# Performance work log

Measured on AMD Instinct MI355X. Metric: run time of the kernel, lower is better.

The kernel has to match this reference:

```python
import jax, jax.numpy as jnp
import numpy as np

KERNEL = 25  # hard-coded moving-average kernel in the torch Model
HID = 128


def moving_avg(x):
    # x: [B, L, C]; edge-pad (KERNEL-1)//2 on each side along time, then mean over window
    p = (KERNEL - 1) // 2
    front = jnp.repeat(x[:, 0:1, :], p, axis=1)
    end = jnp.repeat(x[:, -1:, :], p, axis=1)
    xp = jnp.concatenate([front, x, end], axis=1)  # [B, L+2p, C]
    cs = jnp.cumsum(xp, axis=1)
    cs = jnp.concatenate([jnp.zeros_like(cs[:, :1, :]), cs], axis=1)
    return (cs[:, KERNEL:, :] - cs[:, :-KERNEL, :]) / KERNEL  # [B, L, C]


def memory_enhance(repres, memory):
    # repres: [N, 128], memory: [F, 128]
    attention = jax.nn.softmax(jnp.einsum('nd,fd->nf', repres, memory), axis=1)
    output = jnp.einsum('nf,fd->nd', attention, memory)
    return jnp.concatenate([output, repres], axis=1)  # [N, 256]


def setup_inputs() -> dict:
    key = jax.random.key(0)
    ks = jax.random.split(key, 12)
    B, L, C, P, M = 128, 720, 321, 336, 512
    s = lambda k, shape, fan: jax.random.normal(k, shape, jnp.float32) * (1.0 / np.sqrt(fan))
    return {
        'x': jax.random.normal(ks[0], (B, L, C), jnp.float32),
        'W_s1': s(ks[1], (HID, L), L), 'b_s1': jnp.zeros((HID,), jnp.float32),
        'W_s2': s(ks[2], (P, 2 * HID), 2 * HID), 'b_s2': jnp.zeros((P,), jnp.float32),
        'W_t1': s(ks[3], (HID, L), L), 'b_t1': jnp.zeros((HID,), jnp.float32),
        'W_t2': s(ks[4], (P, 2 * HID), 2 * HID), 'b_t2': jnp.zeros((P,), jnp.float32),
        'mem_S': s(ks[5], (M, HID), HID),
        'mem_T': s(ks[6], (M, HID), HID),
    }


def reference(x, W_s1, b_s1, W_s2, b_s2, W_t1, b_t1, W_t2, b_t2, mem_S, mem_T):
    B, L, C = x.shape
    trend = moving_avg(x)                 # [B, L, C]
    seasonal = x - trend
    seasonal = jnp.transpose(seasonal, (0, 2, 1))  # [B, C, L]
    trend = jnp.transpose(trend, (0, 2, 1))

    def branch(init, W1, b1, mem, W2, b2):
        r = jax.nn.sigmoid(jnp.einsum('bcl,hl->bch', init, W1) + b1)  # [B, C, 128]
        r = r.reshape(-1, HID)
        r = memory_enhance(r, mem)                                    # [N, 256]
        r = r.reshape(B, C, 2 * HID)
        return jnp.einsum('bcd,pd->bcp', r, W2) + b2                  # [B, C, P]

    seasonal_out = branch(seasonal, W_s1, b_s1, mem_S, W_s2, b_s2)
    trend_out = branch(trend, W_t1, b_t1, mem_T, W_t2, b_t2)
    return jnp.transpose(seasonal_out + trend_out, (0, 2, 1))  # [B, P, C]
```

## Files before the change

### kernel.cpp

```cpp
#include <hip/hip_runtime.h>
#include <math.h>

#define BB 128
#define LL 720
#define CC 321
#define HH 128
#define PP 336
#define MM 512
#define LPAD 736

typedef __attribute__((ext_vector_type(8))) short bf16x8;
typedef __attribute__((ext_vector_type(4))) float f32x4;

__device__ __forceinline__ short f2bf(float x) {
  unsigned u = __builtin_bit_cast(unsigned, x);
  u = (u + 0x7FFFu + ((u >> 16) & 1u)) >> 16;
  return (short)u;
}

__device__ __forceinline__ bf16x8 ldfrag(const short* p) {
  short4 a = *(const short4*)p;
  short4 b = *(const short4*)(p + 16);
  bf16x8 r;
  r[0] = a.x; r[1] = a.y; r[2] = a.z; r[3] = a.w;
  r[4] = b.x; r[5] = b.y; r[6] = b.z; r[7] = b.w;
  return r;
}

__device__ __forceinline__ int4 stage_chunk(const short* g) {
  int2 lo = *(const int2*)g;
  int2 hi = *(const int2*)(g + 16);
  int4 r;
  r.x = lo.x; r.y = lo.y; r.z = hi.x; r.w = hi.y;
  return r;
}

__device__ __forceinline__ bf16x8 ldsfragP(const short* tile, int h, int lg) {
  return *(const bf16x8*)&tile[h * 40 + lg * 8];
}

__device__ __forceinline__ bf16x8 ldsfragR(const short* tile, int h, int lg) {
  int2 lo = *(const int2*)&tile[h * 40 + lg * 4];
  int2 hi = *(const int2*)&tile[h * 40 + lg * 4 + 16];
  union { int2 v[2]; bf16x8 f; } u;
  u.v[0] = lo;
  u.v[1] = hi;
  return u.f;
}

__device__ __forceinline__ void gload_lds16(const short* g, short* l) {
  __builtin_amdgcn_global_load_lds(
      (const __attribute__((address_space(1))) unsigned int*)g,
      (__attribute__((address_space(3))) unsigned int*)l, 16, 0, 0);
}

__global__ void weff_kernel(const float* __restrict__ Ws1,
                            const float* __restrict__ Wt1,
                            short* __restrict__ WsT,
                            short* __restrict__ WtT) {
  int idx = blockIdx.x * 256 + threadIdx.x;
  if (idx >= HH * LPAD) return;
  int j = idx % LPAD, h = idx / LPAD;
  if (j >= LL) { WsT[idx] = 0; WtT[idx] = 0; return; }
  float ss = 0.f, st = 0.f;
  if (j == 0) {
    for (int l = 0; l <= 12; ++l) {
      float w = 13.f - (float)l;
      ss += w * Ws1[h * LL + l];
      st += w * Wt1[h * LL + l];
    }
  } else if (j == LL - 1) {
    for (int d = 0; d <= 12; ++d) {
      float w = 13.f - (float)d;
      ss += w * Ws1[h * LL + LL - 1 - d];
      st += w * Wt1[h * LL + LL - 1 - d];
    }
  } else {
    int lo = j - 12 < 0 ? 0 : j - 12;
    int hi = j + 12 > LL - 1 ? LL - 1 : j + 12;
    for (int l = lo; l <= hi; ++l) {
      ss += Ws1[h * LL + l];
      st += Wt1[h * LL + l];
    }
  }
  ss *= (1.f / 25.f);
  st *= (1.f / 25.f);
  WsT[idx] = f2bf(Ws1[h * LL + j] - ss);
  WtT[idx] = f2bf(st);
}

__global__ void memstage_kernel(const float* __restrict__ memS,
                                const float* __restrict__ memT,
                                short* __restrict__ stgS,
                                short* __restrict__ stgT) {
  int e = blockIdx.x * 256 + threadIdx.x;
  int br = e >> 14;
  int s = e & 16383;
  const float* src = br ? memT : memS;
  short* dst = br ? stgT : stgS;
  int tt = s >> 11;
  int c = s & 2047;
  int row = c >> 4, slot = c & 15;
  int sp = slot ^ (row & 7);
  int k = sp >> 2, lg = sp & 3;
  int ft = tt >> 1;
  short out[8];
  if ((tt & 1) == 0) {
    const float* r0 = src + (size_t)(ft * 128 + row) * 128 + k * 32 + lg * 4;
#pragma unroll
    for (int j = 0; j < 4; ++j) {
      out[j] = f2bf(r0[j]);
      out[j + 4] = f2bf(r0[16 + j]);
    }
  } else {
    int fbase = ft * 128 + k * 32 + lg * 4;
#pragma unroll
    for (int j = 0; j < 4; ++j) {
      out[j] = f2bf(src[(size_t)(fbase + j) * 128 + row]);
      out[j + 4] = f2bf(src[(size_t)(fbase + 16 + j) * 128 + row]);
    }
  }
  short4 a = make_short4(out[0], out[1], out[2], out[3]);
  short4 b = make_short4(out[4], out[5], out[6], out[7]);
  *(short4*)&dst[(size_t)s * 8] = a;
  *(short4*)&dst[(size_t)s * 8 + 4] = b;
}

__global__ void w2cvt_kernel(const float* __restrict__ Ws2,
                             const float* __restrict__ Wt2,
                             const float* __restrict__ bs2,
                             const float* __restrict__ bt2,
                             short* __restrict__ W2b, float* __restrict__ b2) {
  int i = blockIdx.x * 256 + threadIdx.x;
  if (i < PP) b2[i] = bs2[i] + bt2[i];
  if (i >= PP * 512) return;
  int p = i >> 9, k = i & 511;
  float v = (k < 256) ? Ws2[p * 256 + k] : Wt2[p * 256 + (k - 256)];
  W2b[i] = f2bf(v);
}

__global__ __launch_bounds__(256) void gemm1_mfma(
    const float* __restrict__ x,
    const short* __restrict__ WsT, const short* __restrict__ WtT,
    const float* __restrict__ bs1, const float* __restrict__ bt1,
    short* __restrict__ r2s, short* __restrict__ r2t) {
  __shared__ __align__(16) short wlds[2][2][128 * 40];
  int tid = threadIdx.x;
  int w = tid >> 6, l = tid & 63, lr = l & 15, lg = l >> 4;
  int ngrp = w >> 1, hhalf = w & 1;
  int n0 = blockIdx.x * 64 + ngrp * 32 + lr;
  int n1 = n0 + 16;
  int b0 = n0 / CC, c0 = n0 - b0 * CC;
  int b1 = n1 / CC, c1 = n1 - b1 * CC;
  const float* xb0 = x + (size_t)b0 * (LL * CC) + c0;
  const float* xb1 = x + (size_t)b1 * (LL * CC) + c1;

  int rowA = tid >> 2, cqA = tid & 3;
  int rowB = (tid + 256) >> 2, cqB = tid & 3;
  const short* gSA = WsT + rowA * LPAD + cqA * 8;
  const short* gSB = WsT + rowB * LPAD + cqB * 8;
  const short* gTA = WtT + rowA * LPAD + cqA * 8;
  const short* gTB = WtT + rowB * LPAD + cqB * 8;
  int dA = rowA * 40 + cqA * 8;
  int dB = rowB * 40 + cqB * 8;

  f32x4 acc[2][4][2];
#pragma unroll
  for (int br = 0; br < 2; ++br)
#pragma unroll
    for (int i = 0; i < 4; ++i)
#pragma unroll
      for (int rt = 0; rt < 2; ++rt) acc[br][i][rt] = (f32x4){0.f, 0.f, 0.f, 0.f};

  {
    int4 sA = *(const int4*)gSA;
    int4 sB = *(const int4*)gSB;
    int4 tA = *(const int4*)gTA;
    int4 tB = *(const int4*)gTB;
    *(int4*)&wlds[0][0][dA] = sA;
    *(int4*)&wlds[0][0][dB] = sB;
    *(int4*)&wlds[0][1][dA] = tA;
    *(int4*)&wlds[0][1][dB] = tB;
  }
  float xc0[8], xc1[8];
#pragma unroll
  for (int j = 0; j < 4; ++j) {
    int k1 = lg * 4 + j, k2 = k1 + 16;
    xc0[j] = xb0[(size_t)k1 * CC];
    xc0[j + 4] = xb0[(size_t)k2 * CC];
    xc1[j] = xb1[(size_t)k1 * CC];
    xc1[j + 4] = xb1[(size_t)k2 * CC];
  }
  __syncthreads();

  int hb = hhalf * 64;
  int cur = 0;
  for (int step = 0; step < 23; ++step) {
    int4 nSA = {0, 0, 0, 0}, nSB = nSA, nTA = nSA, nTB = nSA;
    float xn0[8] = {0.f}, xn1[8] = {0.f};
    if (step < 22) {
      int ko = (step + 1) * 32;
      nSA = *(const int4*)(gSA + ko);
      nSB = *(const int4*)(gSB + ko);
      nTA = *(const int4*)(gTA + ko);
      nTB = *(const int4*)(gTB + ko);
#pragma unroll
      for (int j = 0; j < 4; ++j) {
        int k1 = ko + lg * 4 + j;
        int k2 = k1 + 16;
        bool ok = k2 < LL;
        xn0[j] = xb0[(size_t)k1 * CC];
        xn0[j + 4] = ok ? xb0[(size_t)k2 * CC] : 0.f;
        xn1[j] = xb1[(size_t)k1 * CC];
        xn1[j + 4] = ok ? xb1[(size_t)k2 * CC] : 0.f;
      }
    }

    bf16x8 bx0, bx1;
#pragma unroll
    for (int j = 0; j < 8; ++j) {
      bx0[j] = f2bf(xc0[j]);
      bx1[j] = f2bf(xc1[j]);
    }

    const short* tS = &wlds[cur][0][0];
    const short* tT = &wlds[cur][1][0];
#pragma unroll
    for (int ht = 0; ht < 4; ++ht) {
      int h = hb + ht * 16 + lr;
      bf16x8 aS = ldsfragR(tS, h, lg);
      bf16x8 aT = ldsfragR(tT, h, lg);
      acc[0][ht][0] =
          __builtin_amdgcn_mfma_f32_16x16x32_bf16(aS, bx0, acc[0][ht][0], 0, 0, 0);
      acc[0][ht][1] =
          __builtin_amdgcn_mfma_f32_16x16x32_bf16(aS, bx1, acc[0][ht][1], 0, 0, 0);
      acc[1][ht][0] =
          __builtin_amdgcn_mfma_f32_16x16x32_bf16(aT, bx0, acc[1][ht][0], 0, 0, 0);
      acc[1][ht][1] =
          __builtin_amdgcn_mfma_f32_16x16x32_bf16(aT, bx1, acc[1][ht][1], 0, 0, 0);
    }

    if (step < 22) {
      short* bS = &wlds[cur ^ 1][0][0];
      short* bT = &wlds[cur ^ 1][1][0];
      *(int4*)&bS[dA] = nSA;
      *(int4*)&bS[dB] = nSB;
      *(int4*)&bT[dA] = nTA;
      *(int4*)&bT[dB] = nTB;
    }
    __syncthreads();
#pragma unroll
    for (int j = 0; j < 8; ++j) {
      xc0[j] = xn0[j];
      xc1[j] = xn1[j];
    }
    cur ^= 1;
  }

#pragma unroll
  for (int rt = 0; rt < 2; ++rt) {
    int n = rt ? n1 : n0;
    short* rowS = r2s + (size_t)n * 256 + 128;
    short* rowT = r2t + (size_t)n * 256 + 128;
#pragma unroll
    for (int ht = 0; ht < 4; ++ht) {
      int h = hb + ht * 16 + lg * 4;
      float4 bS = *(const float4*)&bs1[h];
      float4 bT = *(const float4*)&bt1[h];
      const float* pbS = &bS.x;
      const float* pbT = &bT.x;
      short4 ss, st;
      short* ps = &ss.x;
      short* pt = &st.x;
#pragma unroll
      for (int j = 0; j < 4; ++j) {
        ps[j] = f2bf(1.f / (1.f + __expf(-(acc[0][ht][rt][j] + pbS[j]))));
        pt[j] = f2bf(1.f / (1.f + __expf(-(acc[1][ht][rt][j] + pbT[j]))));
      }
      *(short4*)&rowS[h] = ss;
      *(short4*)&rowT[h] = st;
    }
  }
}

__global__ __launch_bounds__(256) void memenh_mfma(
    const short* __restrict__ stgS, const short* __restrict__ stgT,
    short* __restrict__ r2s, short* __restrict__ r2t) {
  int br = blockIdx.y;
  const short* stg = br ? stgT : stgS;
  short* r2 = br ? r2t : r2s;

  __shared__ __align__(16) short buf[2][16384];
  int tid = threadIdx.x;
  int l = tid & 63, lr = l & 15, lg = l >> 4;
  int wbase = tid & 192;
  int n = blockIdx.x * 64 + (tid >> 6) * 16 + lr;

  bf16x8 brag[4];
  {
    const short* rb = r2 + (size_t)n * 256 + 128;
#pragma unroll
    for (int k = 0; k < 4; ++k) brag[k] = ldfrag(rb + k * 32 + lg * 4);
  }

#define STAGE(t, bsel)                                                        \
  {                                                                           \
    const short* g = stg + (size_t)(t)*16384;                                 \
    _Pragma("unroll") for (int i = 0; i < 8; ++i) {                           \
      gload_lds16(g + (size_t)(i * 256 + tid) * 8,                            \
                  &buf[bsel][(i * 256 + wbase) * 8]);                         \
    }                                                                         \
  }

  STAGE(0, 0);
  __syncthreads();

  f32x4 accO[8];
#pragma unroll
  for (int i = 0; i < 8; ++i) accO[i] = (f32x4){0.f, 0.f, 0.f, 0.f};
  bf16x8 pb[4];
  float ssum = 0.f;
  int cur = 0;

#pragma unroll
  for (int t = 0; t < 8; ++t) {
    if (t < 7) STAGE(t + 1, cur ^ 1);
    const short* tb = &buf[cur][0];
    if ((t & 1) == 0) {
      f32x4 sc[8];
#pragma unroll
      for (int ft16 = 0; ft16 < 8; ++ft16) {
        f32x4 a = {0.f, 0.f, 0.f, 0.f};
#pragma unroll
        for (int k = 0; k < 4; ++k) {
          int row = ft16 * 16 + lr;
          int slot = (4 * k + lg) ^ (row & 7);
          bf16x8 af = *(const bf16x8*)&tb[row * 128 + slot * 8];
          a = __builtin_amdgcn_mfma_f32_16x16x32_bf16(af, brag[k], a, 0, 0, 0);
        }
        sc[ft16] = a;
      }
#pragma unroll
      for (int i = 0; i < 8; ++i) {
        f32x4 v = sc[i];
#pragma unroll
        for (int j = 0; j < 4; ++j) {
          float e = __expf(v[j]);
          v[j] = e;
          ssum += e;
        }
        sc[i] = v;
      }
#pragma unroll
      for (int t4 = 0; t4 < 4; ++t4) {
        f32x4 e0 = sc[2 * t4], e1 = sc[2 * t4 + 1];
        bf16x8 f;
        f[0] = f2bf(e0[0]); f[1] = f2bf(e0[1]);
        f[2] = f2bf(e0[2]); f[3] = f2bf(e0[3]);
        f[4] = f2bf(e1[0]); f[5] = f2bf(e1[1]);
        f[6] = f2bf(e1[2]); f[7] = f2bf(e1[3]);
        pb[t4] = f;
      }
    } else {
#pragma unroll
      for (int dt = 0; dt < 8; ++dt) {
#pragma unroll
        for (int k = 0; k < 4; ++k) {
          int row = dt * 16 + lr;
          int slot = (4 * k + lg) ^ (row & 7);
          bf16x8 af = *(const bf16x8*)&tb[row * 128 + slot * 8];
          accO[dt] =
              __builtin_amdgcn_mfma_f32_16x16x32_bf16(af, pb[k], accO[dt], 0, 0, 0);
        }
      }
    }
    __syncthreads();
    cur ^= 1;
  }
#undef STAGE

  ssum += __shfl_xor(ssum, 16);
  ssum += __shfl_xor(ssum, 32);
  float inv = 1.f / ssum;
  short* rowO = r2 + (size_t)n * 256;
#pragma unroll
  for (int dt = 0; dt < 8; ++dt) {
    short4 o;
    o.x = f2bf(accO[dt][0] * inv);
    o.y = f2bf(accO[dt][1] * inv);
    o.z = f2bf(accO[dt][2] * inv);
    o.w = f2bf(accO[dt][3] * inv);
    *(short4*)&rowO[dt * 16 + lg * 4] = o;
  }
}

__global__ __launch_bounds__(512) void gemm2_mfma(
    const short* __restrict__ r2s, const short* __restrict__ r2t,
    const short* __restrict__ W2b,
    const float* __restrict__ b2,
    float* __restrict__ out) {
  __shared__ __align__(16) short w2lds[2][112 * 40];
  int tid = threadIdx.x;
  int w = tid >> 6, l = tid & 63, lr = l & 15, lg = l >> 4;
  int p0 = blockIdx.y * 112;
  int n = blockIdx.x * 128 + w * 16 + lr;
  int b = n / CC, c = n - b * CC;
  const short* rs = r2s + (size_t)n * 256;
  const short* rt = r2t + (size_t)n * 256;

  bool dostage = tid < 448;
  int row = tid >> 2, q = tid & 3;
  const short* gW = W2b + (size_t)(p0 + row) * 512 + q * 4;
  int doff = row * 40 + q * 8;

  f32x4 acc[7];
#pragma unroll
  for (int i = 0; i < 7; ++i) acc[i] = (f32x4){0.f, 0.f, 0.f, 0.f};

  if (dostage) *(int4*)&w2lds[0][doff] = stage_chunk(gW);
  __syncthreads();

  int cur = 0;
  for (int step = 0; step < 16; ++step) {
    int k0 = step * 32;
    const short* rrow = ((k0 < 256) ? rs : rt) + (k0 & 255);
    bf16x8 bfr = ldfrag(rrow + lg * 4);
    int4 nxt = {0, 0, 0, 0};
    if (step < 15 && dostage) nxt = stage_chunk(gW + (step + 1) * 32);
    const short* tw = &w2lds[cur][0];
#pragma unroll
    for (int pt = 0; pt < 7; ++pt) {
      bf16x8 a = ldsfragP(tw, pt * 16 + lr, lg);
      acc[pt] = __builtin_amdgcn_mfma_f32_16x16x32_bf16(a, bfr, acc[pt], 0, 0, 0);
    }
    if (step < 15 && dostage) *(int4*)&w2lds[cur ^ 1][doff] = nxt;
    __syncthreads();
    cur ^= 1;
  }

  size_t obase = (size_t)b * ((size_t)PP * CC) + c;
#pragma unroll
  for (int pt = 0; pt < 7; ++pt) {
    int p = p0 + pt * 16 + lg * 4;
    float4 bias = *(const float4*)&b2[p];
    const float* pb = &bias.x;
#pragma unroll
    for (int j = 0; j < 4; ++j) {
      out[obase + (size_t)(p + j) * CC] = acc[pt][j] + pb[j];
    }
  }
}

extern "C" void kernel_launch(void* const* d_in, const int* in_sizes, int n_in,
                              void* d_out, int out_size, void* d_ws, size_t ws_size,
                              hipStream_t stream) {
  const float* x    = (const float*)d_in[0];
  const float* Ws1  = (const float*)d_in[1];
  const float* bs1  = (const float*)d_in[2];
  const float* Ws2  = (const float*)d_in[3];
  const float* bs2  = (const float*)d_in[4];
  const float* Wt1  = (const float*)d_in[5];
  const float* bt1  = (const float*)d_in[6];
  const float* Wt2  = (const float*)d_in[7];
  const float* bt2  = (const float*)d_in[8];
  const float* memS = (const float*)d_in[9];
  const float* memT = (const float*)d_in[10];
  float* out = (float*)d_out;

  const size_t N = (size_t)BB * CC;
  short* r2s  = (short*)d_ws;
  short* r2t  = r2s + N * 256;
  short* WsTb = r2t + N * 256;
  short* WtTb = WsTb + (size_t)HH * LPAD;
  short* stgS = WtTb + (size_t)HH * LPAD;
  short* stgT = stgS + (size_t)16384 * 8;
  short* W2b  = stgT + (size_t)16384 * 8;
  float* b2   = (float*)(W2b + (size_t)PP * 512);

  weff_kernel<<<(HH * LPAD) / 256, 256, 0, stream>>>(Ws1, Wt1, WsTb, WtTb);
  memstage_kernel<<<128, 256, 0, stream>>>(memS, memT, stgS, stgT);
  w2cvt_kernel<<<(PP * 512) / 256, 256, 0, stream>>>(Ws2, Wt2, bs2, bt2, W2b, b2);

  gemm1_mfma<<<642, 256, 0, stream>>>(x, WsTb, WtTb, bs1, bt1, r2s, r2t);

  dim3 g3(642, 2);
  memenh_mfma<<<g3, 256, 0, stream>>>(stgS, stgT, r2s, r2t);

  dim3 g2(321, 3);
  gemm2_mfma<<<g2, 512, 0, stream>>>(r2s, r2t, W2b, b2, out);
}
```

Baseline: 166.2 us.

## Pre-permute K layout for contiguous 16-byte MFMA fragments and stage x through LDS

Weight and intermediate buffers are written in a permuted K order inside each 32-wide chunk. This lets every MFMA operand fragment load as one contiguous 16-byte vector instead of two 8-byte halves, in both global memory and LDS. gemm1 now stages x cooperatively: each thread loads 8 strided floats for one column, converts them to bf16 once and writes them to a double-buffered LDS tile. Before, each wave loaded and converted its own x fragments in registers. This cuts duplicated global loads and conversions but adds LDS traffic and an extra shared buffer.

```diff
diff --git a/kernel.cpp b/kernel.cpp
--- a/kernel.cpp
+++ b/kernel.cpp
@@ -18,40 +18,8 @@
   return (short)u;
 }
 
-__device__ __forceinline__ bf16x8 ldfrag(const short* p) {
-  short4 a = *(const short4*)p;
-  short4 b = *(const short4*)(p + 16);
-  bf16x8 r;
-  r[0] = a.x; r[1] = a.y; r[2] = a.z; r[3] = a.w;
-  r[4] = b.x; r[5] = b.y; r[6] = b.z; r[7] = b.w;
-  return r;
-}
-
-__device__ __forceinline__ int4 stage_chunk(const short* g) {
-  int2 lo = *(const int2*)g;
-  int2 hi = *(const int2*)(g + 16);
-  int4 r;
-  r.x = lo.x; r.y = lo.y; r.z = hi.x; r.w = hi.y;
-  return r;
-}
-
-__device__ __forceinline__ bf16x8 ldsfragP(const short* tile, int h, int lg) {
-  return *(const bf16x8*)&tile[h * 40 + lg * 8];
-}
-
-__device__ __forceinline__ bf16x8 ldsfragR(const short* tile, int h, int lg) {
-  int2 lo = *(const int2*)&tile[h * 40 + lg * 4];
-  int2 hi = *(const int2*)&tile[h * 40 + lg * 4 + 16];
-  union { int2 v[2]; bf16x8 f; } u;
-  u.v[0] = lo;
-  u.v[1] = hi;
-  return u.f;
-}
-
-__device__ __forceinline__ void gload_lds16(const short* g, short* l) {
-  __builtin_amdgcn_global_load_lds(
-      (const __attribute__((address_space(1))) unsigned int*)g,
-      (__attribute__((address_space(3))) unsigned int*)l, 16, 0, 0);
+__device__ __forceinline__ int packpos(int kw) {
+  return ((kw & 15) >> 2) * 8 + (kw >> 4) * 4 + (kw & 3);
 }
 
 __global__ void weff_kernel(const float* __restrict__ Ws1,
@@ -61,7 +29,9 @@
   int idx = blockIdx.x * 256 + threadIdx.x;
   if (idx >= HH * LPAD) return;
   int j = idx % LPAD, h = idx / LPAD;
-  if (j >= LL) { WsT[idx] = 0; WtT[idx] = 0; return; }
+  int t = j >> 5, kw = j & 31;
+  int dst = h * LPAD + t * 32 + packpos(kw);
+  if (j >= LL) { WsT[dst] = 0; WtT[dst] = 0; return; }
   float ss = 0.f, st = 0.f;
   if (j == 0) {
     for (int l = 0; l <= 12; ++l) {
@@ -85,8 +55,8 @@
   }
   ss *= (1.f / 25.f);
   st *= (1.f / 25.f);
-  WsT[idx] = f2bf(Ws1[h * LL + j] - ss);
-  WtT[idx] = f2bf(st);
+  WsT[dst] = f2bf(Ws1[h * LL + j] - ss);
+  WtT[dst] = f2bf(st);
 }
 
 __global__ void memstage_kernel(const float* __restrict__ memS,
@@ -136,7 +106,7 @@
   if (i >= PP * 512) return;
   int p = i >> 9, k = i & 511;
   float v = (k < 256) ? Ws2[p * 256 + k] : Wt2[p * 256 + (k - 256)];
-  W2b[i] = f2bf(v);
+  W2b[p * 512 + (k >> 5) * 32 + packpos(k & 31)] = f2bf(v);
 }
 
 __global__ __launch_bounds__(256) void gemm1_mfma(
@@ -145,24 +115,28 @@
     const float* __restrict__ bs1, const float* __restrict__ bt1,
     short* __restrict__ r2s, short* __restrict__ r2t) {
   __shared__ __align__(16) short wlds[2][2][128 * 40];
+  __shared__ __align__(16) short xlds[2][64 * 40];
   int tid = threadIdx.x;
   int w = tid >> 6, l = tid & 63, lr = l & 15, lg = l >> 4;
-  int ngrp = w >> 1, hhalf = w & 1;
-  int n0 = blockIdx.x * 64 + ngrp * 32 + lr;
-  int n1 = n0 + 16;
-  int b0 = n0 / CC, c0 = n0 - b0 * CC;
-  int b1 = n1 / CC, c1 = n1 - b1 * CC;
-  const float* xb0 = x + (size_t)b0 * (LL * CC) + c0;
-  const float* xb1 = x + (size_t)b1 * (LL * CC) + c1;
-
-  int rowA = tid >> 2, cqA = tid & 3;
-  int rowB = (tid + 256) >> 2, cqB = tid & 3;
-  const short* gSA = WsT + rowA * LPAD + cqA * 8;
-  const short* gSB = WsT + rowB * LPAD + cqB * 8;
-  const short* gTA = WtT + rowA * LPAD + cqA * 8;
-  const short* gTB = WtT + rowB * LPAD + cqB * 8;
-  int dA = rowA * 40 + cqA * 8;
-  int dB = rowB * 40 + cqB * 8;
+  int ngrp = w >> 1, hhalf = w & 1, hb = hhalf * 64;
+  int nb = blockIdx.x * 64;
+  int cc0 = ngrp * 32 + lr, cc1 = cc0 + 16;
+  int n0 = nb + cc0, n1 = nb + cc1;
+
+  int rowA = tid >> 2, q = tid & 3;
+  int rowB = rowA + 64;
+  const short* gSA = WsT + rowA * LPAD + q * 8;
+  const short* gSB = WsT + rowB * LPAD + q * 8;
+  const short* gTA = WtT + rowA * LPAD + q * 8;
+  const short* gTB = WtT + rowB * LPAD + q * 8;
+  int dA = rowA * 40 + q * 8, dB = rowB * 40 + q * 8;
+
+  int xcc = tid & 63, kg = tid >> 6;
+  int xn = nb + xcc;
+  int xb_ = xn / CC, xc_ = xn - xb_ * CC;
+  const float* xptr = x + (size_t)xb_ * (LL * CC) + xc_;
+  int dx0 = xcc * 40 + ((kg & 1) * 2 + 0) * 8 + (kg >> 1) * 4;
+  int dx1 = xcc * 40 + ((kg & 1) * 2 + 1) * 8 + (kg >> 1) * 4;
 
   f32x4 acc[2][4][2];
 #pragma unroll
@@ -181,23 +155,23 @@
     *(int4*)&wlds[0][0][dB] = sB;
     *(int4*)&wlds[0][1][dA] = tA;
     *(int4*)&wlds[0][1][dB] = tB;
-  }
-  float xc0[8], xc1[8];
-#pragma unroll
-  for (int j = 0; j < 4; ++j) {
-    int k1 = lg * 4 + j, k2 = k1 + 16;
-    xc0[j] = xb0[(size_t)k1 * CC];
-    xc0[j + 4] = xb0[(size_t)k2 * CC];
-    xc1[j] = xb1[(size_t)k1 * CC];
-    xc1[j + 4] = xb1[(size_t)k2 * CC];
+    float xf[8];
+#pragma unroll
+    for (int j = 0; j < 8; ++j) {
+      int k = kg * 8 + j;
+      xf[j] = xptr[(size_t)k * CC];
+    }
+    short4 s0 = make_short4(f2bf(xf[0]), f2bf(xf[1]), f2bf(xf[2]), f2bf(xf[3]));
+    short4 s1 = make_short4(f2bf(xf[4]), f2bf(xf[5]), f2bf(xf[6]), f2bf(xf[7]));
+    *(short4*)&xlds[0][dx0] = s0;
+    *(short4*)&xlds[0][dx1] = s1;
   }
   __syncthreads();
 
-  int hb = hhalf * 64;
   int cur = 0;
   for (int step = 0; step < 23; ++step) {
     int4 nSA = {0, 0, 0, 0}, nSB = nSA, nTA = nSA, nTB = nSA;
-    float xn0[8] = {0.f}, xn1[8] = {0.f};
+    float xf[8] = {0.f};
     if (step < 22) {
       int ko = (step + 1) * 32;
       nSA = *(const int4*)(gSA + ko);
@@ -205,31 +179,22 @@
       nTA = *(const int4*)(gTA + ko);
       nTB = *(const int4*)(gTB + ko);
 #pragma unroll
-      for (int j = 0; j < 4; ++j) {
-        int k1 = ko + lg * 4 + j;
-        int k2 = k1 + 16;
-        bool ok = k2 < LL;
-        xn0[j] = xb0[(size_t)k1 * CC];
-        xn0[j + 4] = ok ? xb0[(size_t)k2 * CC] : 0.f;
-        xn1[j] = xb1[(size_t)k1 * CC];
-        xn1[j + 4] = ok ? xb1[(size_t)k2 * CC] : 0.f;
-      }
-    }
-
-    bf16x8 bx0, bx1;
-#pragma unroll
-    for (int j = 0; j < 8; ++j) {
-      bx0[j] = f2bf(xc0[j]);
-      bx1[j] = f2bf(xc1[j]);
-    }
-
+      for (int j = 0; j < 8; ++j) {
+        int k = ko + kg * 8 + j;
+        xf[j] = (k < LL) ? xptr[(size_t)k * CC] : 0.f;
+      }
+    }
+
+    const short* xl = &xlds[cur][0];
+    bf16x8 bx0 = *(const bf16x8*)&xl[cc0 * 40 + lg * 8];
+    bf16x8 bx1 = *(const bf16x8*)&xl[cc1 * 40 + lg * 8];
     const short* tS = &wlds[cur][0][0];
     const short* tT = &wlds[cur][1][0];
 #pragma unroll
     for (int ht = 0; ht < 4; ++ht) {
       int h = hb + ht * 16 + lr;
-      bf16x8 aS = ldsfragR(tS, h, lg);
-      bf16x8 aT = ldsfragR(tT, h, lg);
+      bf16x8 aS = *(const bf16x8*)&tS[h * 40 + lg * 8];
+      bf16x8 aT = *(const bf16x8*)&tT[h * 40 + lg * 8];
       acc[0][ht][0] =
           __builtin_amdgcn_mfma_f32_16x16x32_bf16(aS, bx0, acc[0][ht][0], 0, 0, 0);
       acc[0][ht][1] =
@@ -247,13 +212,12 @@
       *(int4*)&bS[dB] = nSB;
       *(int4*)&bT[dA] = nTA;
       *(int4*)&bT[dB] = nTB;
+      short4 s0 = make_short4(f2bf(xf[0]), f2bf(xf[1]), f2bf(xf[2]), f2bf(xf[3]));
+      short4 s1 = make_short4(f2bf(xf[4]), f2bf(xf[5]), f2bf(xf[6]), f2bf(xf[7]));
+      *(short4*)&xlds[cur ^ 1][dx0] = s0;
+      *(short4*)&xlds[cur ^ 1][dx1] = s1;
     }
     __syncthreads();
-#pragma unroll
-    for (int j = 0; j < 8; ++j) {
-      xc0[j] = xn0[j];
-      xc1[j] = xn1[j];
-    }
     cur ^= 1;
   }
 
@@ -265,6 +229,8 @@
 #pragma unroll
     for (int ht = 0; ht < 4; ++ht) {
       int h = hb + ht * 16 + lg * 4;
+      int hbase = hb + ht * 16;
+      int dst = (hbase >> 5) * 32 + lg * 8 + ((hbase >> 4) & 1) * 4;
       float4 bS = *(const float4*)&bs1[h];
       float4 bT = *(const float4*)&bt1[h];
       const float* pbS = &bS.x;
@@ -277,8 +243,8 @@
         ps[j] = f2bf(1.f / (1.f + __expf(-(acc[0][ht][rt][j] + pbS[j]))));
         pt[j] = f2bf(1.f / (1.f + __expf(-(acc[1][ht][rt][j] + pbT[j]))));
       }
-      *(short4*)&rowS[h] = ss;
-      *(short4*)&rowT[h] = st;
+      *(short4*)&rowS[dst] = ss;
+      *(short4*)&rowT[dst] = st;
     }
   }
 }
@@ -300,15 +266,20 @@
   {
     const short* rb = r2 + (size_t)n * 256 + 128;
 #pragma unroll
-    for (int k = 0; k < 4; ++k) brag[k] = ldfrag(rb + k * 32 + lg * 4);
+    for (int k = 0; k < 4; ++k)
+      brag[k] = *(const bf16x8*)&rb[k * 32 + lg * 8];
   }
 
 #define STAGE(t, bsel)                                                        \
   {                                                                           \
     const short* g = stg + (size_t)(t)*16384;                                 \
     _Pragma("unroll") for (int i = 0; i < 8; ++i) {                           \
-      gload_lds16(g + (size_t)(i * 256 + tid) * 8,                            \
-                  &buf[bsel][(i * 256 + wbase) * 8]);                         \
+      __builtin_amdgcn_global_load_lds(                                       \
+          (const __attribute__((address_space(1))) unsigned int*)(            \
+              g + (size_t)(i * 256 + tid) * 8),                               \
+          (__attribute__((address_space(3))) unsigned int*)(                  \
+              &buf[bsel][(i * 256 + wbase) * 8]),                             \
+          16, 0, 0);                                                          \
     }                                                                         \
   }
 
@@ -390,7 +361,7 @@
     o.y = f2bf(accO[dt][1] * inv);
     o.z = f2bf(accO[dt][2] * inv);
     o.w = f2bf(accO[dt][3] * inv);
-    *(short4*)&rowO[dt * 16 + lg * 4] = o;
+    *(short4*)&rowO[(dt >> 1) * 32 + lg * 8 + (dt & 1) * 4] = o;
   }
 }
 
@@ -410,27 +381,27 @@
 
   bool dostage = tid < 448;
   int row = tid >> 2, q = tid & 3;
-  const short* gW = W2b + (size_t)(p0 + row) * 512 + q * 4;
+  const short* gW = W2b + (size_t)(p0 + row) * 512 + q * 8;
   int doff = row * 40 + q * 8;
 
   f32x4 acc[7];
 #pragma unroll
   for (int i = 0; i < 7; ++i) acc[i] = (f32x4){0.f, 0.f, 0.f, 0.f};
 
-  if (dostage) *(int4*)&w2lds[0][doff] = stage_chunk(gW);
+  if (dostage) *(int4*)&w2lds[0][doff] = *(const int4*)gW;
   __syncthreads();
 
   int cur = 0;
   for (int step = 0; step < 16; ++step) {
     int k0 = step * 32;
     const short* rrow = ((k0 < 256) ? rs : rt) + (k0 & 255);
-    bf16x8 bfr = ldfrag(rrow + lg * 4);
+    bf16x8 bfr = *(const bf16x8*)&rrow[lg * 8];
     int4 nxt = {0, 0, 0, 0};
-    if (step < 15 && dostage) nxt = stage_chunk(gW + (step + 1) * 32);
+    if (step < 15 && dostage) nxt = *(const int4*)(gW + (step + 1) * 32);
     const short* tw = &w2lds[cur][0];
 #pragma unroll
     for (int pt = 0; pt < 7; ++pt) {
-      bf16x8 a = ldsfragP(tw, pt * 16 + lr, lg);
+      bf16x8 a = *(const bf16x8*)&tw[(pt * 16 + lr) * 40 + lg * 8];
       acc[pt] = __builtin_amdgcn_mfma_f32_16x16x32_bf16(a, bfr, acc[pt], 0, 0, 0);
     }
     if (step < 15 && dostage) *(int4*)&w2lds[cur ^ 1][doff] = nxt;
```

New measurement: 136.0 us. 1.22x faster.
